# Kernel tuning notes

Measured on AMD Instinct MI355X. Metric: run time of the kernel, lower is better.

## Reference

```python
import jax, jax.numpy as jnp
import numpy as np
import math

EPS = 1e-20
TEMP = 0.07


def _affinity(x1, x2, n):
    # x1, x2: (B, C, T-1, N+1); use only the first n (non-dustbin) nodes
    A = jnp.einsum('bctn,bctm->btnm', x1[..., :n], x2[..., :n])  # (B,T-1,n,n)
    # entropy of row-normalized affinities (intended math of Categorical(probs=A[b,t,k]).entropy())
    p = A / A.sum(-1, keepdims=True)
    ent = -(p * jnp.log(jnp.maximum(p, EPS))).sum(-1)            # (B,T-1,n)
    dustbin_w = 1.0 / math.log(n)
    A = jnp.concatenate([A, (ent * dustbin_w)[..., None]], axis=-1)  # (B,T-1,n,n+1)
    dust_row = -A.sum(-2)[:, :, None, :]                              # (B,T-1,1,n+1)
    A = jnp.concatenate([A, dust_row], axis=2)                        # (B,T-1,n+1,n+1)
    A = A.at[:, :, -1, -1].set(0.0)
    return A


def _l2norm(x, axis):
    return x / jnp.maximum(jnp.linalg.norm(x, axis=axis, keepdims=True), 1e-12)


def _forward(feats_raw, dust_raw, W_self, b_self, W_dust, b_dust):
    B, N, Cenc, T = feats_raw.shape
    # selfsim head: Linear over channel dim, then L2-normalize features
    f = jnp.einsum('bnct,cd->bndt', feats_raw, W_self) + b_self[None, None, :, None]
    f = _l2norm(f, axis=2)                      # (B,N,128,T)
    q = jnp.transpose(f, (0, 2, 3, 1))          # (B,128,T,N)
    d = jnp.einsum('bct,cd->bdt', dust_raw, W_dust) + b_dust[None, :, None]
    d = _l2norm(d, axis=1)                      # (B,128,T)
    q = jnp.concatenate([q, d[..., None]], axis=-1)  # (B,128,T,N+1)

    Af = _affinity(q[:, :, :-1], q[:, :, 1:], N)
    qf = jnp.flip(q, axis=2)
    Ab = _affinity(qf[:, :, :-1], qf[:, :, 1:], N)

    A12 = jax.nn.softmax(Af / TEMP, axis=-1)    # (B,T-1,M,M)
    A21 = jax.nn.softmax(Ab / TEMP, axis=-1)

    M = N + 1
    tgt = jnp.tile(jnp.arange(M), B)            # (B*M,)
    rows = jnp.arange(B * M)
    left = A12[:, 0]
    right = A21[:, T - 2]
    losses = []
    for i in range(1, T - 1):                   # fixed small loop over time steps
        left = left @ A12[:, i]
        right = A21[:, T - 2 - i] @ right
        AA = left @ right                       # (B,M,M) palindrome walk
        logits = jnp.log(AA + EPS).reshape(-1, M)
        ls = jax.nn.log_softmax(logits, axis=-1)
        losses.append(-ls[rows, tgt].mean())
    loss = sum(losses) / len(losses)
    return q, loss


def setup_inputs() -> dict:
    key = jax.random.key(0)
    ks = jax.random.split(key, 4)
    B, N, C, T, D = 4, 784, 512, 8, 128
    return {
        'feats_raw': jax.random.normal(ks[0], (B, N, C, T), dtype=jnp.float32),
        'dust_raw': jax.random.normal(ks[1], (B, C, T), dtype=jnp.float32),
        'W_self': jax.random.normal(ks[2], (C, D), dtype=jnp.float32) * 0.05,
        'b_self': jnp.zeros((D,), dtype=jnp.float32),
        'W_dust': jax.random.normal(ks[3], (C, D), dtype=jnp.float32) * 0.05,
        'b_dust': jnp.zeros((D,), dtype=jnp.float32),
    }


def reference(feats_raw, dust_raw, W_self, b_self, W_dust, b_dust):
    return _forward(feats_raw, dust_raw, W_self, b_self, W_dust, b_dust)
```

## Files before the change

kernel.cpp:

```cpp
#include <hip/hip_runtime.h>
#include <hip/hip_bf16.h>
#include <math.h>

constexpr int Bc = 4;
constexpr int Nc = 784;
constexpr int Cc = 512;
constexpr int Tc = 8;
constexpr int Dc = 128;
constexpr int Mc = 785;
constexpr int TM1 = 7;
constexpr int Pp = 832;
constexpr int Qrows = 896;
constexpr float TEMP = 0.07f;

typedef __attribute__((ext_vector_type(4))) float f32x4;
typedef __attribute__((ext_vector_type(8))) unsigned short u16x8;
typedef __attribute__((ext_vector_type(8))) __bf16 bf16x8;

__device__ __forceinline__ unsigned short f2bf(float v) {
    __hip_bfloat16 h = __float2bfloat16(v);
    return __builtin_bit_cast(unsigned short, h);
}
__device__ __forceinline__ float bf2f(unsigned short u) {
    return __builtin_bit_cast(float, (unsigned int)u << 16);
}

__device__ __forceinline__ void gload16(const void* g, void* l) {
    __builtin_amdgcn_global_load_lds(
        (const __attribute__((address_space(1))) unsigned int*)g,
        (__attribute__((address_space(3))) unsigned int*)l, 16, 0, 0);
}

template<int LD>
__device__ __forceinline__ void gemm64x128_db(const unsigned short* __restrict__ A,
                                              const unsigned short* __restrict__ BT,
                                              unsigned short* As0, unsigned short* As1,
                                              unsigned short* Bs0, unsigned short* Bs1,
                                              int i0, int j0, int tid, f32x4 (&acc)[4][2])
{
    const int lane = tid & 63, wv = tid >> 6;
    const int g = lane >> 4, lr = lane & 15;
    constexpr int NT = LD / 64;

    #pragma unroll
    for (int q = 0; q < 2; ++q) {
        int s = q * 256 + tid; int r = s >> 3;
        int csw = ((s & 7) << 4) ^ ((r & 7) << 4);
        gload16((const char*)(A + (size_t)(i0 + r) * LD) + csw, As0 + (size_t)s * 8);
    }
    #pragma unroll
    for (int q = 0; q < 4; ++q) {
        int s = q * 256 + tid; int r = s >> 3;
        int csw = ((s & 7) << 4) ^ ((r & 7) << 4);
        gload16((const char*)(BT + (size_t)(j0 + r) * LD) + csw, Bs0 + (size_t)s * 8);
    }
    __syncthreads();

    for (int t = 0; t < NT; ++t) {
        unsigned short* Asc = (t & 1) ? As1 : As0;
        unsigned short* Bsc = (t & 1) ? Bs1 : Bs0;
        if (t + 1 < NT) {
            int k0 = (t + 1) * 64;
            unsigned short* Asn = (t & 1) ? As0 : As1;
            unsigned short* Bsn = (t & 1) ? Bs0 : Bs1;
            #pragma unroll
            for (int q = 0; q < 2; ++q) {
                int s = q * 256 + tid; int r = s >> 3;
                int csw = ((s & 7) << 4) ^ ((r & 7) << 4);
                gload16((const char*)(A + (size_t)(i0 + r) * LD + k0) + csw, Asn + (size_t)s * 8);
            }
            #pragma unroll
            for (int q = 0; q < 4; ++q) {
                int s = q * 256 + tid; int r = s >> 3;
                int csw = ((s & 7) << 4) ^ ((r & 7) << 4);
                gload16((const char*)(BT + (size_t)(j0 + r) * LD + k0) + csw, Bsn + (size_t)s * 8);
            }
        }
        bf16x8 af[2][4], bf[2][2];
        #pragma unroll
        for (int ks = 0; ks < 2; ++ks) {
            #pragma unroll
            for (int m = 0; m < 4; ++m) {
                int r = m * 16 + lr;
                int cb = (ks * 64 + g * 16) ^ ((r & 7) << 4);
                af[ks][m] = __builtin_bit_cast(bf16x8, *(const u16x8*)((const char*)Asc + r * 128 + cb));
            }
            #pragma unroll
            for (int n = 0; n < 2; ++n) {
                int r = wv * 32 + n * 16 + lr;
                int cb = (ks * 64 + g * 16) ^ ((r & 7) << 4);
                bf[ks][n] = __builtin_bit_cast(bf16x8, *(const u16x8*)((const char*)Bsc + r * 128 + cb));
            }
        }
        #pragma unroll
        for (int ks = 0; ks < 2; ++ks)
            #pragma unroll
            for (int m = 0; m < 4; ++m)
                #pragma unroll
                for (int n = 0; n < 2; ++n)
                    acc[m][n] = __builtin_amdgcn_mfma_f32_16x16x32_bf16(af[ks][m], bf[ks][n], acc[m][n], 0, 0, 0);
        __syncthreads();
    }
}

__device__ __forceinline__ float blockReduceSum(float v, float* sbuf) {
    #pragma unroll
    for (int off = 32; off; off >>= 1) v += __shfl_down(v, off, 64);
    __syncthreads();
    if ((threadIdx.x & 63) == 0) sbuf[threadIdx.x >> 6] = v;
    __syncthreads();
    return sbuf[0] + sbuf[1] + sbuf[2] + sbuf[3];
}
__device__ __forceinline__ float blockReduceMax(float v, float* sbuf) {
    #pragma unroll
    for (int off = 32; off; off >>= 1) v = fmaxf(v, __shfl_down(v, off, 64));
    __syncthreads();
    if ((threadIdx.x & 63) == 0) sbuf[threadIdx.x >> 6] = v;
    __syncthreads();
    return fmaxf(fmaxf(sbuf[0], sbuf[1]), fmaxf(sbuf[2], sbuf[3]));
}

__global__ __launch_bounds__(256) void k_pack(const float* __restrict__ feats,
                                              const float* __restrict__ Wself,
                                              const float* __restrict__ Wdust,
                                              unsigned int* __restrict__ Abf32,
                                              unsigned short* __restrict__ WTb,
                                              unsigned short* __restrict__ qTb,
                                              float* __restrict__ csR,
                                              float* __restrict__ loss)
{
    __shared__ float lds[Cc * 9];
    int bid = blockIdx.x;
    int tid = threadIdx.x;
    if (bid >= Bc * Nc + 32) {
        int zb = bid - (Bc * Nc + 32);
        if (zb == 0) {
            int n = 6 * Bc * Pp;
            for (int i = tid; i < n; i += 256) csR[i] = 0.f;
            if (tid == 0) *loss = 0.f;
        }
        u16x8 z = {};
        for (int bt = zb * 4; bt < zb * 4 + 4; ++bt) {
            u16x8* dst = (u16x8*)(qTb + ((size_t)bt * Qrows + Nc) * Dc);
            for (int i = tid; i < (Qrows - Nc) * Dc / 8; i += 256) dst[i] = z;
        }
        return;
    }
    if (bid >= Bc * Nc) {
        int pidx = bid - Bc * Nc;
        int which = pidx >> 4;
        int rem = pidx & 15;
        int d0 = (rem >> 3) * 64, c0 = (rem & 7) * 64;
        const float* W = which ? Wdust : Wself;
        unsigned short* O = WTb + (size_t)which * Dc * Cc;
        int tx = tid & 63, ty = tid >> 6;
        #pragma unroll
        for (int y = 0; y < 64; y += 4) lds[(y + ty) * 65 + tx] = W[(size_t)(c0 + y + ty) * Dc + d0 + tx];
        __syncthreads();
        #pragma unroll
        for (int y = 0; y < 64; y += 4) O[(size_t)(d0 + y + ty) * Cc + c0 + tx] = f2bf(lds[tx * 65 + y + ty]);
        return;
    }
    int b = bid / Nc, n = bid % Nc;
    const float* src = feats + (size_t)(b * Nc + n) * Cc * Tc;
    for (int i = tid; i < Cc * Tc; i += 256) lds[(i >> 3) * 9 + (i & 7)] = src[i];
    __syncthreads();
    #pragma unroll
    for (int t = 0; t < Tc; ++t) {
        size_t row = (size_t)(b * Tc + t) * Nc + n;
        float v0 = lds[(2 * tid) * 9 + t];
        float v1 = lds[(2 * tid + 1) * 9 + t];
        unsigned int pk = (unsigned int)f2bf(v0) | ((unsigned int)f2bf(v1) << 16);
        Abf32[row * (Cc / 2) + tid] = pk;
    }
}

__global__ __launch_bounds__(256, 3) void k_gemm_proj(const unsigned short* __restrict__ A,
                                                      const unsigned short* __restrict__ BT,
                                                      const float* __restrict__ bias,
                                                      float* __restrict__ Cf)
{
    __shared__ __align__(16) unsigned short As0[64 * 64], As1[64 * 64];
    __shared__ __align__(16) unsigned short Bs0[128 * 64], Bs1[128 * 64];
    const int i0 = blockIdx.x * 64;
    const int tid = threadIdx.x, lane = tid & 63, wv = tid >> 6;
    const int g = lane >> 4, lr = lane & 15;

    f32x4 acc[4][2] = {};
    gemm64x128_db<Cc>(A, BT, As0, As1, Bs0, Bs1, i0, 0, tid, acc);

    #pragma unroll
    for (int n = 0; n < 2; ++n) {
        int col = wv * 32 + n * 16 + lr;
        float bv = bias[col];
        #pragma unroll
        for (int m = 0; m < 4; ++m)
            #pragma unroll
            for (int j = 0; j < 4; ++j) {
                int row = i0 + m * 16 + g * 4 + j;
                Cf[(size_t)row * Dc + col] = acc[m][n][j] + bv;
            }
    }
}

__global__ __launch_bounds__(256) void k_norm(const float* __restrict__ fbuf,
                                              const float* __restrict__ dust,
                                              const float* __restrict__ Wdust,
                                              const float* __restrict__ bdust,
                                              unsigned short* __restrict__ qTb,
                                              float* __restrict__ qout)
{
    __shared__ float lds[64][129];
    __shared__ float nrm[64][4];
    __shared__ float inv[64];
    __shared__ float red2[2];
    int bt = blockIdx.y;
    int b = bt >> 3, t = bt & 7;
    int tid = threadIdx.x;

    if (blockIdx.x == 13) {
        float* sdust = &lds[0][0];
        for (int i = tid; i < Cc; i += 256) sdust[i] = dust[((size_t)b * Cc + i) * Tc + t];
        __syncthreads();
        float acc = 0.f;
        if (tid < 128) {
            for (int c = 0; c < Cc; ++c) acc += sdust[c] * Wdust[(size_t)c * Dc + tid];
            acc += bdust[tid];
            float s = acc * acc;
            #pragma unroll
            for (int off = 32; off; off >>= 1) s += __shfl_down(s, off, 64);
            if ((tid & 63) == 0) red2[tid >> 6] = s;
        }
        __syncthreads();
        if (tid < 128) {
            float inv0 = 1.f / fmaxf(sqrtf(red2[0] + red2[1]), 1e-12f);
            float qv = acc * inv0;
            qout[(((size_t)b * Dc + tid) * Tc + t) * Mc + Nc] = qv;
        }
        return;
    }

    int n0 = blockIdx.x * 64;
    #pragma unroll
    for (int q = 0; q < 8; ++q) {
        int i = q * 256 + tid;
        int nl = i >> 5, d4 = i & 31;
        f32x4 v = {};
        if (n0 + nl < Nc) v = *(const f32x4*)(fbuf + ((size_t)bt * Nc + n0 + nl) * Dc + d4 * 4);
        *(f32x4*)(&lds[nl][d4 * 4]) = v;
    }
    __syncthreads();
    {
        int r = tid & 63, p = tid >> 6;
        float s = 0.f;
        #pragma unroll
        for (int j = 0; j < 32; ++j) { float v = lds[r][p * 32 + j]; s += v * v; }
        nrm[r][p] = s;
    }
    __syncthreads();
    if (tid < 64) inv[tid] = 1.f / fmaxf(sqrtf(nrm[tid][0] + nrm[tid][1] + nrm[tid][2] + nrm[tid][3]), 1e-12f);
    __syncthreads();
    unsigned int* qT32 = (unsigned int*)(qTb + (size_t)bt * Qrows * Dc);
    #pragma unroll
    for (int q = 0; q < 16; ++q) {
        int i = q * 256 + tid;
        int nl = i >> 6, dp = i & 63;
        if (n0 + nl < Nc) {
            float iv = inv[nl];
            unsigned int pk = (unsigned int)f2bf(lds[nl][2 * dp] * iv)
                            | ((unsigned int)f2bf(lds[nl][2 * dp + 1] * iv) << 16);
            qT32[((size_t)(n0 + nl) * Dc >> 1) + dp] = pk;
        }
    }
    int nl = tid & 63;
    if (n0 + nl < Nc) {
        float iv = inv[nl];
        #pragma unroll
        for (int dd = 0; dd < Dc; dd += 4) {
            int d = dd + (tid >> 6);
            qout[(((size_t)b * Dc + d) * Tc + t) * Mc + n0 + nl] = lds[nl][d] * iv;
        }
    }
}

__global__ __launch_bounds__(256, 2) void k_affinity(const unsigned short* __restrict__ qTb,
                                                     unsigned short* __restrict__ P12h,
                                                     unsigned short* __restrict__ P21h,
                                                     float* __restrict__ cs12,
                                                     float* __restrict__ cs21,
                                                     float wconst)
{
    constexpr float INVT = 1.0f / TEMP;
    const size_t MMp = (size_t)Pp * Pp;
    __shared__ unsigned short otile[16][840];
    __shared__ float sred[16][4][2];
    __shared__ float rowsum[16], invZ[16], entP[16];

    int f = blockIdx.x;
    int xcd = f & 7, slot = f >> 3;
    int grp = xcd + 8 * (slot / 49);
    int strip = slot % 49;
    int side = grp >= 28 ? 1 : 0;
    int bt = grp - side * 28;
    int b = bt / TM1, t = bt % TM1;
    const unsigned short *Aq, *Bq;
    unsigned short* OUT;
    if (side == 0) {
        Aq = qTb + (size_t)(b * Tc + t)     * Qrows * Dc;
        Bq = qTb + (size_t)(b * Tc + t + 1) * Qrows * Dc;
        OUT = P12h + (size_t)bt * MMp;
    } else {
        Aq = qTb + (size_t)(b * Tc + 7 - t) * Qrows * Dc;
        Bq = qTb + (size_t)(b * Tc + 6 - t) * Qrows * Dc;
        OUT = P21h + (size_t)bt * MMp;
    }
    float* csFlip = (side == 0 ? cs21 : cs12) + (size_t)(b * TM1 + (6 - t)) * Pp;

    const int r0 = strip * 16;
    const int tid = threadIdx.x, lane = tid & 63, w = tid >> 6;
    const int g = lane >> 4, lr = lane & 15;

    f32x4 acc[13] = {};
    #pragma unroll
    for (int ks = 0; ks < 4; ++ks) {
        bf16x8 af = __builtin_bit_cast(bf16x8,
            *(const u16x8*)(Aq + (size_t)(r0 + lr) * Dc + ks * 32 + g * 8));
        bf16x8 bfr[13];
        #pragma unroll
        for (int tt = 0; tt < 13; ++tt)
            bfr[tt] = __builtin_bit_cast(bf16x8,
                *(const u16x8*)(Bq + (size_t)((w * 13 + tt) * 16 + lr) * Dc + ks * 32 + g * 8));
        #pragma unroll
        for (int tt = 0; tt < 13; ++tt)
            acc[tt] = __builtin_amdgcn_mfma_f32_16x16x32_bf16(af, bfr[tt], acc[tt], 0, 0, 0);
    }

    float rs[4] = {0.f, 0.f, 0.f, 0.f};
    #pragma unroll
    for (int tt = 0; tt < 13; ++tt) {
        #pragma unroll
        for (int j = 0; j < 4; ++j) rs[j] += acc[tt][j];
    }
    #pragma unroll
    for (int off = 1; off <= 8; off <<= 1) {
        #pragma unroll
        for (int j = 0; j < 4; ++j) rs[j] += __shfl_xor(rs[j], off, 64);
    }
    if (lr == 0) {
        #pragma unroll
        for (int j = 0; j < 4; ++j) sred[g * 4 + j][w][0] = rs[j];
    }
    __syncthreads();
    if (tid < 16) {
        float r = sred[tid][0][0] + sred[tid][1][0] + sred[tid][2][0] + sred[tid][3][0];
        rowsum[tid] = r;
        csFlip[r0 + tid] = r;
    }
    __syncthreads();

    float invr[4];
    #pragma unroll
    for (int j = 0; j < 4; ++j) invr[j] = 1.0f / rowsum[g * 4 + j];
    const float padc = (w == 3) ? 3.0f : 0.0f;
    float en[4] = {0.f, 0.f, 0.f, 0.f}, es[4] = {0.f, 0.f, 0.f, 0.f};
    #pragma unroll
    for (int tt = 0; tt < 13; ++tt) {
        #pragma unroll
        for (int j = 0; j < 4; ++j) {
            float a = acc[tt][j];
            float e = __expf(a * INVT);
            es[j] += e;
            float p = a * invr[j];
            en[j] -= p * __logf(fmaxf(p, 1e-20f));
            acc[tt][j] = e;
        }
    }
    #pragma unroll
    for (int j = 0; j < 4; ++j) es[j] -= padc;
    #pragma unroll
    for (int off = 1; off <= 8; off <<= 1) {
        #pragma unroll
        for (int j = 0; j < 4; ++j) {
            es[j] += __shfl_xor(es[j], off, 64);
            en[j] += __shfl_xor(en[j], off, 64);
        }
    }
    if (lr == 0) {
        #pragma unroll
        for (int j = 0; j < 4; ++j) { sred[g * 4 + j][w][0] = es[j]; sred[g * 4 + j][w][1] = en[j]; }
    }
    __syncthreads();
    if (tid < 16) {
        float esum = sred[tid][0][0] + sred[tid][1][0] + sred[tid][2][0] + sred[tid][3][0];
        float ent  = sred[tid][0][1] + sred[tid][1][1] + sred[tid][2][1] + sred[tid][3][1];
        float ez  = __expf(ent * wconst * INVT);
        float Z   = esum + ez;
        float iz  = 1.0f / Z;
        invZ[tid] = iz;
        entP[tid] = ez * iz;
    }
    __syncthreads();

    float izl[4];
    #pragma unroll
    for (int j = 0; j < 4; ++j) izl[j] = invZ[g * 4 + j];
    #pragma unroll
    for (int tt = 0; tt < 13; ++tt) {
        int gt = w * 13 + tt;
        int col = gt * 16 + lr;
        #pragma unroll
        for (int j = 0; j < 4; ++j) {
            float v = acc[tt][j] * izl[j];
            if (gt >= 49) v = 0.f;
            otile[g * 4 + j][col] = f2bf(v);
        }
    }
    __syncthreads();
    if (tid < 16) otile[tid][784] = f2bf(entP[tid]);
    __syncthreads();

    for (int v = tid; v < 16 * 104; v += 256) {
        int row = v / 104, cv = v % 104;
        *(u16x8*)(OUT + (size_t)(r0 + row) * Pp + cv * 8) = *(const u16x8*)(&otile[row][cv * 8]);
    }
}

__global__ __launch_bounds__(256) void k_dustrow(const float* __restrict__ cs12,
                                                 const float* __restrict__ cs21,
                                                 unsigned short* __restrict__ P12h,
                                                 unsigned short* __restrict__ P21h)
{
    constexpr float INVT = 1.0f / TEMP;
    const size_t MMp = (size_t)Pp * Pp;
    int bt = blockIdx.x, side = blockIdx.y;
    const float* cs = (side ? cs21 : cs12) + (size_t)bt * Pp;
    unsigned short* OUT = (side ? P21h : P12h) + (size_t)bt * MMp;
    __shared__ float sbuf[4];
    int tid = threadIdx.x;
    float v[4];
    #pragma unroll
    for (int k = 0; k < 4; ++k) {
        int j = tid + k * 256;
        float val = -INFINITY;
        if (j < Nc)       val = -cs[j] * INVT;
        else if (j == Nc) val = 0.f;
        v[k] = val;
    }
    float mx = fmaxf(fmaxf(v[0], v[1]), fmaxf(v[2], v[3]));
    mx = blockReduceMax(mx, sbuf);
    float e[4]; float s = 0.f;
    #pragma unroll
    for (int k = 0; k < 4; ++k) {
        int j = tid + k * 256;
        e[k] = (j < Mc) ? __expf(v[k] - mx) : 0.f;
        s += e[k];
    }
    s = blockReduceSum(s, sbuf);
    float invs = 1.f / s;
    #pragma unroll
    for (int k = 0; k < 4; ++k) {
        int j = tid + k * 256;
        if (j < Mc)      OUT[(size_t)Nc * Pp + j] = f2bf(e[k] * invs);
        else if (j < Pp) OUT[(size_t)Nc * Pp + j] = 0;
    }
    u16x8 z = {};
    u16x8* dst = (u16x8*)(OUT + (size_t)785 * Pp);
    for (int i = tid; i < (Pp - 785) * Pp / 8; i += 256) dst[i] = z;
}

__global__ __launch_bounds__(256) void k_transpose_bf16(const unsigned short* __restrict__ P12h,
                                                        const unsigned short* __restrict__ P21h,
                                                        unsigned short* __restrict__ Db)
{
    const size_t MMp = (size_t)Pp * Pp;
    __shared__ unsigned short tile[64][65];
    int z = blockIdx.z;
    const unsigned short* S;
    if (z < 24) { int b = z / 6, tm = z % 6; S = P12h + ((size_t)b * 7 + tm + 1) * MMp; }
    else        { S = P21h + ((size_t)(z - 24) * 7 + 6) * MMp; }
    unsigned short* D = Db + (size_t)z * MMp;
    int x0 = blockIdx.x * 64, y0 = blockIdx.y * 64;
    int tx = threadIdx.x & 63, ty = threadIdx.x >> 6;
    #pragma unroll
    for (int y = 0; y < 64; y += 4) tile[y + ty][tx] = S[(size_t)(y0 + y + ty) * Pp + x0 + tx];
    __syncthreads();
    #pragma unroll
    for (int y = 0; y < 64; y += 4) D[(size_t)(x0 + y + ty) * Pp + y0 + tx] = tile[tx][y + ty];
}

struct GJobs {
    const unsigned short* A[2];
    const unsigned short* BT[2];
    unsigned short* Cb[2];
    float* cs[2];
    long long sA[2], sB[2], sC[2];
    const unsigned short* Lr;
    const unsigned short* Rr;
    const float* csL;
    float* loss;
    float scale;
};

__global__ __launch_bounds__(256, 3) void k_gemm_loss(GJobs J)
{
    const size_t MMp = (size_t)Pp * Pp;
    if (blockIdx.x >= 728) {
        int q = blockIdx.x - 728;
        int w = threadIdx.x >> 6, lane = threadIdx.x & 63;
        int r = q * 4 + w;
        int b = r / Mc, i = r % Mc;
        const u16x8* lrow = (const u16x8*)(J.Lr + (size_t)b * MMp + (size_t)i * Pp);
        const u16x8* rrow = (const u16x8*)(J.Rr + (size_t)b * MMp + (size_t)i * Pp);
        const f32x4* cs4  = (const f32x4*)(J.csL + (size_t)b * Pp);
        float sR = 0.f, sD = 0.f;
        for (int c = lane; c < Pp / 8; c += 64) {
            u16x8 lv = lrow[c];
            u16x8 rv = rrow[c];
            f32x4 c0 = cs4[2 * c], c1 = cs4[2 * c + 1];
            #pragma unroll
            for (int k = 0; k < 4; ++k) {
                float fl = bf2f(lv[k]);
                sR += fl * c0[k];
                sD += fl * bf2f(rv[k]);
            }
            #pragma unroll
            for (int k = 0; k < 4; ++k) {
                float fl = bf2f(lv[4 + k]);
                sR += fl * c1[k];
                sD += fl * bf2f(rv[4 + k]);
            }
        }
        #pragma unroll
        for (int off = 1; off <= 32; off <<= 1) {
            sR += __shfl_xor(sR, off, 64);
            sD += __shfl_xor(sD, off, 64);
        }
        if (lane == 0)
            atomicAdd(J.loss, (logf(sR + Mc * 1e-20f) - logf(sD + 1e-20f)) * J.scale);
        return;
    }

    __shared__ __align__(16) unsigned short As0[64 * 64], As1[64 * 64];
    __shared__ __align__(16) unsigned short Bs0[128 * 64], Bs1[128 * 64];

    int f = blockIdx.x;
    int zz = f & 7, slot = f >> 3;
    int job = zz >> 2, b = zz & 3;
    const unsigned short* A  = J.A[job]  + (size_t)b * J.sA[job];
    const unsigned short* BT = J.BT[job] + (size_t)b * J.sB[job];

    const int i0 = (slot / 7) * 64, j0 = (slot % 7) * 128;
    const int tid = threadIdx.x, lane = tid & 63, wv = tid >> 6;
    const int g = lane >> 4, lr = lane & 15;

    f32x4 acc[4][2] = {};
    gemm64x128_db<Pp>(A, BT, As0, As1, Bs0, Bs1, i0, j0, tid, acc);

    unsigned short* Co = J.Cb[job] + (size_t)b * J.sC[job];
    float* csp = J.cs[job];
    float csacc[2] = {0.f, 0.f};
    #pragma unroll
    for (int m = 0; m < 4; ++m)
        #pragma unroll
        for (int n = 0; n < 2; ++n)
            #pragma unroll
            for (int j = 0; j < 4; ++j) {
                int row = i0 + m * 16 + g * 4 + j;
                int col = j0 + wv * 32 + n * 16 + lr;
                if (col < Pp) {
                    unsigned short h = f2bf(acc[m][n][j]);
                    Co[(size_t)row * Pp + col] = h;
                    csacc[n] += bf2f(h);
                }
            }
    if (csp) {
        csp += (size_t)b * Pp;
        #pragma unroll
        for (int n = 0; n < 2; ++n) {
            float p = csacc[n];
            p += __shfl_xor(p, 16, 64);
            p += __shfl_xor(p, 32, 64);
            int col = j0 + wv * 32 + n * 16 + lr;
            if (g == 0 && col < Pp) atomicAdd(&csp[col], p);
        }
    }
}

__global__ __launch_bounds__(64) void k_lossrow(const unsigned short* __restrict__ L,
                                                const unsigned short* __restrict__ R,
                                                const float* __restrict__ csR,
                                                float* __restrict__ loss, float scale)
{
    const size_t MMp = (size_t)Pp * Pp;
    int r = blockIdx.x;
    int b = r / Mc, i = r % Mc;
    const u16x8* lrow = (const u16x8*)(L + (size_t)b * MMp + (size_t)i * Pp);
    const u16x8* rrow = (const u16x8*)(R + (size_t)b * MMp + (size_t)i * Pp);
    const f32x4* cs4  = (const f32x4*)(csR + (size_t)b * Pp);
    int lane = threadIdx.x;
    float sR = 0.f, sD = 0.f;
    for (int c = lane; c < Pp / 8; c += 64) {
        u16x8 lv = lrow[c];
        u16x8 rv = rrow[c];
        f32x4 c0 = cs4[2 * c], c1 = cs4[2 * c + 1];
        #pragma unroll
        for (int k = 0; k < 4; ++k) {
            float fl = bf2f(lv[k]);
            sR += fl * c0[k];
            sD += fl * bf2f(rv[k]);
        }
        #pragma unroll
        for (int k = 0; k < 4; ++k) {
            float fl = bf2f(lv[4 + k]);
            sR += fl * c1[k];
            sD += fl * bf2f(rv[4 + k]);
        }
    }
    #pragma unroll
    for (int off = 1; off <= 32; off <<= 1) {
        sR += __shfl_xor(sR, off, 64);
        sD += __shfl_xor(sD, off, 64);
    }
    if (lane == 0)
        atomicAdd(loss, (logf(sR + Mc * 1e-20f) - logf(sD + 1e-20f)) * scale);
}

extern "C" void kernel_launch(void* const* d_in, const int* in_sizes, int n_in,
                              void* d_out, int out_size, void* d_ws, size_t ws_size,
                              hipStream_t stream)
{
    const float* feats = (const float*)d_in[0];
    const float* dust  = (const float*)d_in[1];
    const float* Wself = (const float*)d_in[2];
    const float* bself = (const float*)d_in[3];
    const float* Wdust = (const float*)d_in[4];
    const float* bdust = (const float*)d_in[5];

    float* out  = (float*)d_out;
    float* qout = out;
    float* loss = out + (size_t)Bc * Dc * Tc * Mc;

    const size_t MMp = (size_t)Pp * Pp;

    float* ws = (float*)d_ws;
    float* csR = ws;
    unsigned short* P12h = (unsigned short*)(ws + 4 * MMp);
    unsigned short* P21h = P12h + (size_t)28 * MMp;
    unsigned short* chainT = P21h + (size_t)28 * MMp;
    unsigned short* P12T  = chainT;
    unsigned short* P21T6 = P12T + (size_t)24 * MMp;
    unsigned short* l0    = P21T6 + (size_t)4 * MMp;
    unsigned short* l1    = l0 + (size_t)4 * MMp;
    unsigned short* R0    = l1 + (size_t)4 * MMp;
    unsigned short* R1    = R0 + (size_t)4 * MMp;
    unsigned short* qTb   = R1 + (size_t)4 * MMp;
    float* cs12 = (float*)(qTb + (size_t)32 * Qrows * Dc);
    float* cs21 = cs12 + (size_t)28 * Pp;

    unsigned short* Abf   = chainT;
    unsigned int*   Abf32 = (unsigned int*)Abf;
    unsigned short* WTb   = Abf + (size_t)Bc * Tc * Nc * Cc;
    float*          fbuf  = (float*)(WTb + 2 * (size_t)Dc * Cc);

    k_pack<<<Bc * Nc + 32 + 8, 256, 0, stream>>>(feats, Wself, Wdust, Abf32, WTb, qTb, csR, loss);
    k_gemm_proj<<<392, 256, 0, stream>>>(Abf, WTb, bself, fbuf);
    k_norm<<<dim3(14, 32), 256, 0, stream>>>(fbuf, dust, Wdust, bdust, qTb, qout);
    float wconst = (float)(1.0 / log(784.0));
    k_affinity<<<2744, 256, 0, stream>>>(qTb, P12h, P21h, cs12, cs21, wconst);
    k_dustrow<<<dim3(28, 2), 256, 0, stream>>>(cs12, cs21, P12h, P21h);
    k_transpose_bf16<<<dim3(13, 13, 28), 256, 0, stream>>>(P12h, P21h, P12T);

    const float scale = 1.0f / (6.0f * Bc * Mc);

    {
        GJobs J = {};
        J.A[0] = P12h;  J.sA[0] = (long long)7 * MMp;
        J.BT[0] = P12T; J.sB[0] = (long long)6 * MMp;
        J.Cb[0] = l0;   J.sC[0] = (long long)MMp; J.cs[0] = nullptr;
        J.A[1] = P21T6;                   J.sA[1] = (long long)MMp;
        J.BT[1] = P21h + (size_t)5 * MMp; J.sB[1] = (long long)7 * MMp;
        J.Cb[1] = R0;   J.sC[1] = (long long)MMp; J.cs[1] = csR;
        k_gemm_loss<<<728, 256, 0, stream>>>(J);
    }

    unsigned short *lcur = l0, *lnxt = l1, *rcur = R0, *rnxt = R1;
    for (int i = 1; i <= 5; ++i) {
        GJobs J = {};
        J.A[0] = lcur; J.sA[0] = (long long)MMp;
        J.BT[0] = P12T + (size_t)i * MMp; J.sB[0] = (long long)6 * MMp;
        J.Cb[0] = lnxt; J.sC[0] = (long long)MMp; J.cs[0] = nullptr;
        J.A[1] = rcur; J.sA[1] = (long long)MMp;
        J.BT[1] = P21h + (size_t)(5 - i) * MMp; J.sB[1] = (long long)7 * MMp;
        J.Cb[1] = rnxt; J.sC[1] = (long long)MMp; J.cs[1] = csR + (size_t)i * Bc * Pp;
        J.Lr = lcur; J.Rr = rcur; J.csL = csR + (size_t)(i - 1) * Bc * Pp;
        J.loss = loss; J.scale = scale;
        k_gemm_loss<<<728 + 785, 256, 0, stream>>>(J);
        unsigned short* t;
        t = lcur; lcur = lnxt; lnxt = t;
        t = rcur; rcur = rnxt; rnxt = t;
    }
    k_lossrow<<<Bc * Mc, 64, 0, stream>>>(lcur, rcur, csR + (size_t)5 * Bc * Pp, loss, scale);
}
```

Baseline: 435.2 us.

## Pair forward and backward affinity tiles sharing the same B operand per block

The affinity kernel now assigns to each block a pair of (A, B) products that share the same B time slice. The block loads B fragments once and runs MFMAs against two A row strips, so grid size falls from 2744 to 1568 blocks and redundant global loads of B are avoided. The cost is doubled accumulator registers; the occupancy hint of 2 in the launch bounds was dropped, so occupancy may fall. The softmax/entropy epilogue also runs twice serially per block, reusing shared memory.

```diff
diff --git a/kernel.cpp b/kernel.cpp
--- a/kernel.cpp
+++ b/kernel.cpp
@@ -283,58 +283,16 @@
     }
 }
 
-__global__ __launch_bounds__(256, 2) void k_affinity(const unsigned short* __restrict__ qTb,
-                                                     unsigned short* __restrict__ P12h,
-                                                     unsigned short* __restrict__ P21h,
-                                                     float* __restrict__ cs12,
-                                                     float* __restrict__ cs21,
-                                                     float wconst)
+__device__ __forceinline__ void aff_process(f32x4 (&acc)[13],
+                                            unsigned short* __restrict__ OUT,
+                                            float* __restrict__ csFlip,
+                                            int r0, int tid, int w, int g, int lr,
+                                            float wconst,
+                                            unsigned short (*otile)[840],
+                                            float (*sred)[4][2],
+                                            float* rowsum, float* invZ, float* entP)
 {
     constexpr float INVT = 1.0f / TEMP;
-    const size_t MMp = (size_t)Pp * Pp;
-    __shared__ unsigned short otile[16][840];
-    __shared__ float sred[16][4][2];
-    __shared__ float rowsum[16], invZ[16], entP[16];
-
-    int f = blockIdx.x;
-    int xcd = f & 7, slot = f >> 3;
-    int grp = xcd + 8 * (slot / 49);
-    int strip = slot % 49;
-    int side = grp >= 28 ? 1 : 0;
-    int bt = grp - side * 28;
-    int b = bt / TM1, t = bt % TM1;
-    const unsigned short *Aq, *Bq;
-    unsigned short* OUT;
-    if (side == 0) {
-        Aq = qTb + (size_t)(b * Tc + t)     * Qrows * Dc;
-        Bq = qTb + (size_t)(b * Tc + t + 1) * Qrows * Dc;
-        OUT = P12h + (size_t)bt * MMp;
-    } else {
-        Aq = qTb + (size_t)(b * Tc + 7 - t) * Qrows * Dc;
-        Bq = qTb + (size_t)(b * Tc + 6 - t) * Qrows * Dc;
-        OUT = P21h + (size_t)bt * MMp;
-    }
-    float* csFlip = (side == 0 ? cs21 : cs12) + (size_t)(b * TM1 + (6 - t)) * Pp;
-
-    const int r0 = strip * 16;
-    const int tid = threadIdx.x, lane = tid & 63, w = tid >> 6;
-    const int g = lane >> 4, lr = lane & 15;
-
-    f32x4 acc[13] = {};
-    #pragma unroll
-    for (int ks = 0; ks < 4; ++ks) {
-        bf16x8 af = __builtin_bit_cast(bf16x8,
-            *(const u16x8*)(Aq + (size_t)(r0 + lr) * Dc + ks * 32 + g * 8));
-        bf16x8 bfr[13];
-        #pragma unroll
-        for (int tt = 0; tt < 13; ++tt)
-            bfr[tt] = __builtin_bit_cast(bf16x8,
-                *(const u16x8*)(Bq + (size_t)((w * 13 + tt) * 16 + lr) * Dc + ks * 32 + g * 8));
-        #pragma unroll
-        for (int tt = 0; tt < 13; ++tt)
-            acc[tt] = __builtin_amdgcn_mfma_f32_16x16x32_bf16(af, bfr[tt], acc[tt], 0, 0, 0);
-    }
-
     float rs[4] = {0.f, 0.f, 0.f, 0.f};
     #pragma unroll
     for (int tt = 0; tt < 13; ++tt) {
@@ -423,6 +381,75 @@
         int row = v / 104, cv = v % 104;
         *(u16x8*)(OUT + (size_t)(r0 + row) * Pp + cv * 8) = *(const u16x8*)(&otile[row][cv * 8]);
     }
+}
+
+__global__ __launch_bounds__(256) void k_affinity(const unsigned short* __restrict__ qTb,
+                                                  unsigned short* __restrict__ P12h,
+                                                  unsigned short* __restrict__ P21h,
+                                                  float* __restrict__ cs12,
+                                                  float* __restrict__ cs21,
+                                                  float wconst)
+{
+    const size_t MMp = (size_t)Pp * Pp;
+    __shared__ unsigned short otile[16][840];
+    __shared__ float sred[16][4][2];
+    __shared__ float rowsum[16], invZ[16], entP[16];
+
+    int f = blockIdx.x;
+    int xcd = f & 7, slot = f >> 3;
+    int grp = xcd + 8 * (slot / 49);
+    int strip = slot % 49;
+    int b = grp >> 3, k = grp & 7;
+    bool pairb = (k < 6);
+
+    int tB = (k < 6) ? (k + 1) : ((k == 6) ? 7 : 0);
+    const unsigned short* Bq = qTb + (size_t)(b * Tc + tB) * Qrows * Dc;
+
+    const unsigned short* Aq0;
+    unsigned short* OUT0;
+    float* cs0;
+    if (k <= 6) {
+        Aq0 = qTb + (size_t)(b * Tc + k) * Qrows * Dc;
+        OUT0 = P12h + (size_t)(b * TM1 + k) * MMp;
+        cs0  = cs21 + (size_t)(b * TM1 + (6 - k)) * Pp;
+    } else {
+        Aq0 = qTb + (size_t)(b * Tc + 1) * Qrows * Dc;
+        OUT0 = P21h + (size_t)(b * TM1 + 6) * MMp;
+        cs0  = cs12 + (size_t)(b * TM1 + 0) * Pp;
+    }
+    const unsigned short* Aq1 = qTb + (size_t)(b * Tc + k + 2) * Qrows * Dc;
+    unsigned short* OUT1 = P21h + (size_t)(b * TM1 + (5 - k)) * MMp;
+    float* cs1 = cs12 + (size_t)(b * TM1 + (k + 1)) * Pp;
+
+    const int r0 = strip * 16;
+    const int tid = threadIdx.x, lane = tid & 63, w = tid >> 6;
+    const int g = lane >> 4, lr = lane & 15;
+
+    f32x4 acc0[13] = {}, acc1[13] = {};
+    #pragma unroll
+    for (int ks = 0; ks < 4; ++ks) {
+        bf16x8 af0 = __builtin_bit_cast(bf16x8,
+            *(const u16x8*)(Aq0 + (size_t)(r0 + lr) * Dc + ks * 32 + g * 8));
+        bf16x8 bfr[13];
+        #pragma unroll
+        for (int tt = 0; tt < 13; ++tt)
+            bfr[tt] = __builtin_bit_cast(bf16x8,
+                *(const u16x8*)(Bq + (size_t)((w * 13 + tt) * 16 + lr) * Dc + ks * 32 + g * 8));
+        #pragma unroll
+        for (int tt = 0; tt < 13; ++tt)
+            acc0[tt] = __builtin_amdgcn_mfma_f32_16x16x32_bf16(af0, bfr[tt], acc0[tt], 0, 0, 0);
+        if (pairb) {
+            bf16x8 af1 = __builtin_bit_cast(bf16x8,
+                *(const u16x8*)(Aq1 + (size_t)(r0 + lr) * Dc + ks * 32 + g * 8));
+            #pragma unroll
+            for (int tt = 0; tt < 13; ++tt)
+                acc1[tt] = __builtin_amdgcn_mfma_f32_16x16x32_bf16(af1, bfr[tt], acc1[tt], 0, 0, 0);
+        }
+    }
+
+    aff_process(acc0, OUT0, cs0, r0, tid, w, g, lr, wconst, otile, sred, rowsum, invZ, entP);
+    if (pairb)
+        aff_process(acc1, OUT1, cs1, r0, tid, w, g, lr, wconst, otile, sred, rowsum, invZ, entP);
 }
 
 __global__ __launch_bounds__(256) void k_dustrow(const float* __restrict__ cs12,
@@ -666,7 +693,7 @@
     k_gemm_proj<<<392, 256, 0, stream>>>(Abf, WTb, bself, fbuf);
     k_norm<<<dim3(14, 32), 256, 0, stream>>>(fbuf, dust, Wdust, bdust, qTb, qout);
     float wconst = (float)(1.0 / log(784.0));
-    k_affinity<<<2744, 256, 0, stream>>>(qTb, P12h, P21h, cs12, cs21, wconst);
+    k_affinity<<<1568, 256, 0, stream>>>(qTb, P12h, P21h, cs12, cs21, wconst);
     k_dustrow<<<dim3(28, 2), 256, 0, stream>>>(cs12, cs21, P12h, P21h);
     k_transpose_bf16<<<dim3(13, 13, 28), 256, 0, stream>>>(P12h, P21h, P12T);
 
```

New measurement: 477.7 us. +9.8%, slower.
